# Optimization experiments

Hardware: AMD Instinct MI355X
Metric: run time of the kernel (lower is better)

Reference implementation:

```python
import jax, jax.numpy as jnp
import numpy as np

B, S, D, H = 2, 2048, 1024, 16
HD = D // H


def setup_inputs() -> dict:
    key = jax.random.key(0)
    ks = jax.random.split(key, 6)
    std = 1.0 / np.sqrt(D)
    return {
        "hidden_states": jax.random.normal(ks[0], (B, S, D), dtype=jnp.float32),
        "attention_mask": jnp.zeros((B, 1, S, S), dtype=jnp.float32),
        "Wq": jax.random.normal(ks[1], (D, D), dtype=jnp.float32) * std,
        "bq": jnp.zeros((D,), dtype=jnp.float32),
        "Wk": jax.random.normal(ks[2], (D, D), dtype=jnp.float32) * std,
        "bk": jnp.zeros((D,), dtype=jnp.float32),
        "Wv": jax.random.normal(ks[3], (D, D), dtype=jnp.float32) * std,
        "bv": jnp.zeros((D,), dtype=jnp.float32),
        "Wo": jax.random.normal(ks[4], (D, D), dtype=jnp.float32) * std,
        "bo": jnp.zeros((D,), dtype=jnp.float32),
    }


def reference(hidden_states, attention_mask, Wq, bq, Wk, bk, Wv, bv, Wo, bo):
    scale = HD ** (-0.5)
    # torch Linear: y = x @ W^T + b
    def proj(x, W, b):
        y = jnp.einsum('bsd,ed->bse', x, W) + b
        return y.reshape(B, S, H, HD).transpose(0, 2, 1, 3)  # [B,H,S,HD]
    q = proj(hidden_states, Wq, bq)
    k = proj(hidden_states, Wk, bk)
    v = proj(hidden_states, Wv, bv)
    scores = jnp.einsum('bhqd,bhkd->bhqk', q, k) * scale + attention_mask
    attn = jax.nn.softmax(scores, axis=-1)  # dropout p=0.0 -> identity
    out = jnp.einsum('bhqk,bhkd->bhqd', attn, v)
    out = out.transpose(0, 2, 1, 3).reshape(B, S, D)
    return jnp.einsum('bsd,ed->bse', out, Wo) + bo
```

## Files before the change

kernel.cpp:

```cpp
#include <hip/hip_runtime.h>
#include <hip/hip_bf16.h>
#include <stdint.h>

#define Bb 2
#define Ss 2048
#define Dd 1024
#define Hh 16
#define HD 64

typedef __attribute__((ext_vector_type(8))) __bf16 bf16x8;
typedef __attribute__((ext_vector_type(4))) __bf16 bf16x4;
typedef __attribute__((ext_vector_type(2))) __bf16 bf16x2;
typedef __attribute__((ext_vector_type(4))) float f32x4;
typedef __attribute__((ext_vector_type(16))) float f32x16;

#define LOG2E 1.44269504088896f
#define SCL2 (0.125f * LOG2E)

#define HS_N   (Bb * Ss * Dd)
#define W_N    (Dd * Dd)
#define B_N    (Dd)
#define MS_N   ((long)Bb * Ss * Ss)
#define CAN_HS 0
#define CAN_WQ (CAN_HS + HS_N)
#define CAN_BQ (CAN_WQ + W_N)
#define CAN_WK (CAN_BQ + B_N)
#define CAN_BK (CAN_WK + W_N)
#define CAN_WV (CAN_BK + B_N)
#define CAN_BV (CAN_WV + W_N)
#define CAN_WO (CAN_BV + B_N)
#define CAN_BO (CAN_WO + W_N)
#define CAN_END (CAN_BO + B_N)
#define TSZ    (Bb * Hh * Ss * HD)
#define WS_ELEMS (CAN_END + 4 * TSZ)
#define WS_NEED ((size_t)WS_ELEMS * 2)

__device__ __forceinline__ void gl_lds16(const __bf16* g, __bf16* l) {
  __builtin_amdgcn_global_load_lds(
      (const __attribute__((address_space(1))) void*)g,
      (__attribute__((address_space(3))) void*)l,
      16, 0, 0);
}

__device__ __forceinline__ void cfence() { asm volatile("" ::: "memory"); }

__global__ void canon_kernel(const float* hs, const float* Wq, const float* bq,
                             const float* Wk, const float* bk, const float* Wv,
                             const float* bv, const float* Wo, const float* bo,
                             __bf16* __restrict__ dst) {
  const float* srcs[9] = {hs, Wq, bq, Wk, bk, Wv, bv, Wo, bo};
  const long starts[10] = {CAN_HS, CAN_WQ, CAN_BQ, CAN_WK, CAN_BK,
                           CAN_WV, CAN_BV, CAN_WO, CAN_BO, CAN_END};
  const long nA = CAN_END / 8;
  for (long c = blockIdx.x * blockDim.x + threadIdx.x; c < nA;
       c += (long)gridDim.x * blockDim.x) {
    const long i = c * 8;
    int seg = 0;
#pragma unroll
    for (int t = 1; t < 9; t++) seg += (i >= starts[t]) ? 1 : 0;
    const float* s = srcs[seg] + (i - starts[seg]);
    bf16x8 v;
#pragma unroll
    for (int e = 0; e < 8; e++) v[e] = (__bf16)s[e];
    *(bf16x8*)(dst + i) = v;
  }
}

template <int MODE, typename OutT>
__global__ __launch_bounds__(256, 3) void gemm_bt(
    const __bf16* __restrict__ A,
    const __bf16* __restrict__ W0, const __bf16* __restrict__ W1,
    const __bf16* __restrict__ W2,
    const __bf16* __restrict__ b0, const __bf16* __restrict__ b1,
    const __bf16* __restrict__ b2,
    OutT* __restrict__ O0, OutT* __restrict__ O1, OutT* __restrict__ O2,
    const float* __restrict__ Mf, __bf16* __restrict__ Mout) {
  constexpr int TN = (MODE == 1) ? 64 : 128;
  constexpr int NACC = TN / 32;
  __shared__ __align__(16) __bf16 sA[2][128 * 32];
  __shared__ __align__(16) __bf16 sB[2][TN * 32];
  const int tid = threadIdx.x;

  if (MODE == 0 && blockIdx.y >= 24) {
    const long nC = MS_N / 8;
    const long c0 = ((long)(blockIdx.y - 24) * 32 + blockIdx.x) * 256 + tid;
    for (long c = c0; c < nC; c += 65536) {
      const float* s = Mf + c * 8;
      bf16x8 v;
#pragma unroll
      for (int e = 0; e < 8; e++) v[e] = (__bf16)(s[e] * LOG2E);
      *(bf16x8*)(Mout + c * 8) = v;
    }
    return;
  }

  const int lane = tid & 63;
  const int wid = tid >> 6;
  const int quad = lane >> 4;
  const int l15 = lane & 15;
  const int mBlock = blockIdx.x * 128;

  const __bf16* W;
  const __bf16* bias;
  OutT* Out;
  int nBlock, which = 0;
  if (MODE == 0) {
    which = blockIdx.y >> 3;
    nBlock = (blockIdx.y & 7) * 128;
    W = which == 0 ? W0 : (which == 1 ? W1 : W2);
    bias = which == 0 ? b0 : (which == 1 ? b1 : b2);
    Out = which == 0 ? O0 : (which == 1 ? O1 : O2);
  } else {
    nBlock = blockIdx.y * TN;
    W = W0;
    bias = b0;
    Out = O0;
  }

  const int waveM = (wid >> 1) * 64;
  const int waveN = (wid & 1) * (TN / 2);

  f32x4 acc[4][NACC] = {};

  const int c1 = wid * 64 + lane;
  const int c2 = c1 + 256;
  const __bf16* Ar1 = A + (mBlock + (c1 >> 2)) * Dd + (c1 & 3) * 8;
  const __bf16* Ar2 = A + (mBlock + (c2 >> 2)) * Dd + (c2 & 3) * 8;
  const __bf16* Wr1 = W + (nBlock + (c1 >> 2)) * Dd + (c1 & 3) * 8;
  const __bf16* Wr2 = W + (nBlock + (c2 >> 2)) * Dd + (c2 & 3) * 8;
  const int d1 = (wid * 64) * 8;
  const int d2 = (wid * 64 + 256) * 8;

#define GSTAGE(BI, K0)                                                        \
  {                                                                           \
    gl_lds16(Ar1 + (K0), sA[BI] + d1);                                        \
    gl_lds16(Ar2 + (K0), sA[BI] + d2);                                        \
    gl_lds16(Wr1 + (K0), sB[BI] + d1);                                        \
    if (MODE == 0) gl_lds16(Wr2 + (K0), sB[BI] + d2);                         \
  }

  GSTAGE(0, 0);

#pragma unroll 2
  for (int kt = 0; kt < 32; ++kt) {
    const int bufc = kt & 1;
    __syncthreads();
    if (kt < 31) {
      GSTAGE(bufc ^ 1, (kt + 1) * 32);
    }

    bf16x8 aF[4], bF[NACC];
#pragma unroll
    for (int mi = 0; mi < 4; mi++)
      aF[mi] =
          *(const bf16x8*)(sA[bufc] + (waveM + mi * 16 + l15) * 32 + quad * 8);
#pragma unroll
    for (int ni = 0; ni < NACC; ni++)
      bF[ni] =
          *(const bf16x8*)(sB[bufc] + (waveN + ni * 16 + l15) * 32 + quad * 8);
#pragma unroll
    for (int mi = 0; mi < 4; mi++)
#pragma unroll
      for (int ni = 0; ni < NACC; ni++)
        acc[mi][ni] = __builtin_amdgcn_mfma_f32_16x16x32_bf16(
            aF[mi], bF[ni], acc[mi][ni], 0, 0, 0);
  }

#pragma unroll
  for (int ni = 0; ni < NACC; ni++) {
    const int ng = nBlock + waveN + ni * 16 + l15;
    const float bv = (float)bias[ng];
#pragma unroll
    for (int mi = 0; mi < 4; mi++) {
      const int mg0 = mBlock + waveM + mi * 16 + quad * 4;
      if (MODE == 0 && which == 2) {
        const int b = mg0 >> 11, s0 = mg0 & 2047;
        const int h = ng >> 6, hd = ng & 63;
        bf16x4 pk;
#pragma unroll
        for (int r = 0; r < 4; r++) pk[r] = (__bf16)(acc[mi][ni][r] + bv);
        *(bf16x4*)((__bf16*)Out + (((b * Hh + h) * HD + hd) * Ss) + s0) = pk;
      } else {
#pragma unroll
        for (int r = 0; r < 4; r++) {
          float v = acc[mi][ni][r] + bv;
          const int m = mg0 + r;
          if (MODE == 0) {
            if (which == 0) v *= SCL2;
            const int b = m >> 11, s = m & 2047;
            const int h = ng >> 6, hd = ng & 63;
            Out[(((b * Hh + h) * Ss + s) * HD) + hd] = (OutT)v;
          } else {
            Out[m * Dd + ng] = (OutT)v;
          }
        }
      }
    }
  }
}

__global__ __launch_bounds__(256, 4) void attn_fused(
    const __bf16* __restrict__ Qg, const __bf16* __restrict__ Kg,
    const __bf16* __restrict__ Vt, const __bf16* __restrict__ Mbf,
    __bf16* __restrict__ Og) {
  __shared__ __align__(16) union {
    struct {
      __bf16 kv[2][8192];
      __bf16 mk[4096];
    } s;
    struct {
      float O[2][64][32];
      float L[2][32];
    } m;
  } sh;

  const int tid = threadIdx.x;
  const int lane = tid & 63;
  const int wid = tid >> 6;
  const int qg = wid & 1;
  const int kvh = wid >> 1;
  const int l31 = lane & 31;
  const int hi = lane >> 5;

  const int id = blockIdx.x;
  const int j = id >> 3;
  const int bh = (id & 7) * 4 + (j >> 5);
  const int qb0 = (j & 31) * 64;
  const int b = bh >> 4;
  const int h = bh & 15;
  const int qw = qb0 + qg * 32 + l31;

  const __bf16* Qp = Qg + (size_t)bh * Ss * HD;
  const __bf16* Kp = Kg + (size_t)bh * Ss * HD;
  const __bf16* Vp = Vt + (size_t)bh * HD * Ss;
  const __bf16* Mb = Mbf + (size_t)b * Ss * Ss;

  bf16x8 qf[4];
#pragma unroll
  for (int k = 0; k < 4; k++)
    qf[k] = *(const bf16x8*)(Qp + (size_t)qw * HD + k * 16 + hi * 8);

  const int cA = tid, cB = 256 + tid;
#define STAGE_KV(BI, KVS)                                                     \
  {                                                                           \
    const int rwA = (cA & 255) >> 2, rwB = (cB & 255) >> 2;                   \
    const int slA = (cA & 3) ^ ((rwA >> 1) & 3);                              \
    const int slB = (cB & 3) ^ ((rwB >> 1) & 3);                              \
    __bf16* kb = sh.s.kv[BI];                                                 \
    gl_lds16(Kp + ((KVS) + rwA) * HD + (cA >> 8) * 32 + slA * 8, kb + cA * 8);\
    gl_lds16(Kp + ((KVS) + rwB) * HD + (cB >> 8) * 32 + slB * 8, kb + cB * 8);\
    __bf16* vb = sh.s.kv[BI] + 4096;                                          \
    gl_lds16(Vp + (size_t)rwA * Ss + (KVS) + (cA >> 8) * 32 + slA * 8,        \
             vb + cA * 8);                                                    \
    gl_lds16(Vp + (size_t)rwB * Ss + (KVS) + (cB >> 8) * 32 + slB * 8,        \
             vb + cB * 8);                                                    \
  }

#define STAGE_M(KVS)                                                          \
  {                                                                           \
    _Pragma("unroll")                                                         \
    for (int rr = 0; rr < 2; rr++) {                                          \
      const int c = tid + rr * 256;                                           \
      const int mq = c >> 3;                                                  \
      const int l8 = (c & 7) ^ (mq & 7);                                      \
      gl_lds16(Mb + (size_t)(qb0 + mq) * Ss + (KVS) + l8 * 8,                 \
               sh.s.mk + c * 8);                                              \
    }                                                                         \
  }

  f32x16 o[2] = {};
  f32x4 lacc = {0.f, 0.f, 0.f, 0.f};

  const int rsw = (l31 >> 1) & 3;

  STAGE_KV(0, 0);
  STAGE_M(0);

  for (int it = 0; it < 32; ++it) {
    const int bufc = it & 1;
    cfence();
    asm volatile("s_waitcnt vmcnt(0)" ::: "memory");
    cfence();
    __builtin_amdgcn_s_barrier();
    cfence();
    if (it < 31) {
      STAGE_KV(bufc ^ 1, (it + 1) * 64);
      cfence();
    }

    bf16x4 mcv[4];
    const int mq = qg * 32 + l31;
#pragma unroll
    for (int g = 0; g < 4; g++) {
      const int p8 = (4 * kvh + g) ^ (l31 & 7);
      mcv[g] = *(const bf16x4*)(sh.s.mk + mq * 64 + p8 * 8 + 4 * hi);
    }
    cfence();
    asm volatile("s_waitcnt lgkmcnt(0)" ::: "memory");
    cfence();
    __builtin_amdgcn_s_barrier();
    cfence();
    if (it < 31) {
      STAGE_M((it + 1) * 64);
      cfence();
    }

    f32x16 sacc;
#pragma unroll
    for (int g = 0; g < 4; g++)
#pragma unroll
      for (int r = 0; r < 4; r++) sacc[g * 4 + r] = (float)mcv[g][r];
    __builtin_amdgcn_s_setprio(1);
#pragma unroll
    for (int k = 0; k < 4; k++) {
      const int ps = (((k & 1) << 1) | hi) ^ rsw;
      bf16x8 kf = *(const bf16x8*)(sh.s.kv[bufc] +
                                   ((k >> 1) * 64 + kvh * 32 + l31) * 32 +
                                   ps * 8);
      sacc = __builtin_amdgcn_mfma_f32_32x32x16_bf16(kf, qf[k], sacc, 0, 0, 0);
    }
    __builtin_amdgcn_s_setprio(0);

    f32x4 sv[4];
#pragma unroll
    for (int g = 0; g < 4; g++)
#pragma unroll
      for (int r = 0; r < 4; r++)
        sv[g][r] = __builtin_amdgcn_exp2f(sacc[g * 4 + r]);
    lacc += (sv[0] + sv[1]) + (sv[2] + sv[3]);

    union pu { bf16x4 v; uint32_t w[2]; };
    pu pk[4];
#pragma unroll
    for (int g = 0; g < 4; g++)
#pragma unroll
      for (int r = 0; r < 4; r++) pk[g].v[r] = (__bf16)sv[g][r];
    union PF { bf16x8 v; uint32_t u[4]; } pf[2];
#pragma unroll
    for (int ks = 0; ks < 2; ks++) {
      uint32_t a0 = pk[2 * ks].w[0], b0 = pk[2 * ks + 1].w[0];
      uint32_t a1 = pk[2 * ks].w[1], b1 = pk[2 * ks + 1].w[1];
      asm volatile("s_nop 1\n\tv_permlane32_swap_b32 %0, %1"
                   : "+v"(a0), "+v"(b0));
      asm volatile("s_nop 1\n\tv_permlane32_swap_b32 %0, %1"
                   : "+v"(a1), "+v"(b1));
      pf[ks].u[0] = a0;
      pf[ks].u[1] = a1;
      pf[ks].u[2] = b0;
      pf[ks].u[3] = b1;
    }

    __builtin_amdgcn_s_setprio(1);
#pragma unroll
    for (int k = 0; k < 2; k++)
#pragma unroll
      for (int hb = 0; hb < 2; hb++) {
        const int ps = ((k << 1) | hi) ^ rsw;
        bf16x8 vf = *(const bf16x8*)(sh.s.kv[bufc] + 4096 +
                                     (kvh * 64 + hb * 32 + l31) * 32 +
                                     ps * 8);
        o[hb] = __builtin_amdgcn_mfma_f32_32x32x16_bf16(vf, pf[k].v, o[hb],
                                                        0, 0, 0);
      }
    __builtin_amdgcn_s_setprio(0);
  }

  float l = lacc[0] + lacc[1] + lacc[2] + lacc[3];
  l += __shfl_xor(l, 32);

  __syncthreads();
  if (kvh == 1) {
#pragma unroll
    for (int hb = 0; hb < 2; hb++)
#pragma unroll
      for (int r = 0; r < 16; r++) {
        const int hd = hb * 32 + (r & 3) + 8 * (r >> 2) + 4 * hi;
        sh.m.O[qg][hd][l31] = o[hb][r];
      }
    if (hi == 0) sh.m.L[qg][l31] = l;
  }
  __syncthreads();
  if (kvh == 0) {
#pragma unroll
    for (int hb = 0; hb < 2; hb++)
#pragma unroll
      for (int r = 0; r < 16; r++) {
        const int hd = hb * 32 + (r & 3) + 8 * (r >> 2) + 4 * hi;
        o[hb][r] += sh.m.O[qg][hd][l31];
      }
    l += sh.m.L[qg][l31];
    const float inv = 1.0f / l;
    __bf16* Ow = Og + (((size_t)b * Ss + qw) * Hh + h) * HD;
#pragma unroll
    for (int hb = 0; hb < 2; hb++)
#pragma unroll
      for (int g = 0; g < 4; g++) {
        const int hd = hb * 32 + g * 8 + 4 * hi;
        bf16x2 w0, w1;
        w0[0] = (__bf16)(o[hb][g * 4 + 0] * inv);
        w0[1] = (__bf16)(o[hb][g * 4 + 1] * inv);
        w1[0] = (__bf16)(o[hb][g * 4 + 2] * inv);
        w1[1] = (__bf16)(o[hb][g * 4 + 3] * inv);
        *(bf16x2*)(Ow + hd) = w0;
        *(bf16x2*)(Ow + hd + 2) = w1;
      }
  }
}

extern "C" void kernel_launch(void* const* d_in, const int* in_sizes, int n_in,
                              void* d_out, int out_size, void* d_ws,
                              size_t ws_size, hipStream_t stream) {
  if (ws_size < WS_NEED) return;

  __bf16* ws = (__bf16*)d_ws;
  const __bf16* hsC = ws + CAN_HS;
  const __bf16* WqC = ws + CAN_WQ;
  const __bf16* bqC = ws + CAN_BQ;
  const __bf16* WkC = ws + CAN_WK;
  const __bf16* bkC = ws + CAN_BK;
  const __bf16* WvC = ws + CAN_WV;
  const __bf16* bvC = ws + CAN_BV;
  const __bf16* WoC = ws + CAN_WO;
  const __bf16* boC = ws + CAN_BO;
  __bf16* Q = ws + CAN_END;
  __bf16* K = Q + TSZ;
  __bf16* V = K + TSZ;
  __bf16* AW = V + TSZ;
  float* out = (float*)d_out;
  __bf16* Mbf = (__bf16*)d_out;

  canon_kernel<<<2048, 256, 0, stream>>>(
      (const float*)d_in[0], (const float*)d_in[2], (const float*)d_in[3],
      (const float*)d_in[4], (const float*)d_in[5], (const float*)d_in[6],
      (const float*)d_in[7], (const float*)d_in[8], (const float*)d_in[9], ws);
  gemm_bt<0, __bf16><<<dim3(32, 32), 256, 0, stream>>>(
      hsC, WqC, WkC, WvC, bqC, bkC, bvC, Q, K, V, (const float*)d_in[1], Mbf);
  gemm_bt<0, __bf16><<<dim3(32, 24), 256, 0, stream>>>(
      hsC, WqC, WkC, WvC, bqC, bkC, bvC, Q, K, V, (const float*)d_in[1], Mbf);
  attn_fused<<<dim3(1024), 256, 0, stream>>>(Q, K, V, Mbf, AW);
  gemm_bt<1, float><<<dim3(32, 16), 256, 0, stream>>>(
      AW, WoC, WoC, WoC, boC, boC, boC, out, out, out, nullptr, nullptr);
}
```

Baseline: 265.0 us.

## Pre-tile mask into MFMA fragment order and load it directly to registers

The mask conversion now writes the bf16 mask in a per-tile layout that matches each lane's MFMA accumulator fragment. The attention kernel can then load its mask values with two vector global loads per iteration, prefetched one tile ahead, instead of staging them through LDS. This removes the LDS mask buffer, one barrier and an lgkmcnt wait per iteration. A redundant second launch of the QKV projection kernel is also removed. The trade-off is more registers for the prefetched mask and scattered writes in the conversion kernel.

```diff
diff --git a/kernel.cpp b/kernel.cpp
--- a/kernel.cpp
+++ b/kernel.cpp
@@ -85,11 +85,23 @@
     const long nC = MS_N / 8;
     const long c0 = ((long)(blockIdx.y - 24) * 32 + blockIdx.x) * 256 + tid;
     for (long c = c0; c < nC; c += 65536) {
-      const float* s = Mf + c * 8;
-      bf16x8 v;
-#pragma unroll
-      for (int e = 0; e < 8; e++) v[e] = (__bf16)(s[e] * LOG2E);
-      *(bf16x8*)(Mout + c * 8) = v;
+      const long i = c * 8;
+      const int b = (int)(i >> 22);
+      const int q = (int)((i >> 11) & 2047);
+      const int kv = (int)(i & 2047);
+      const float* s = Mf + i;
+      const int qt = q >> 6, qg = (q >> 5) & 1, l31 = q & 31;
+      const int kvt = kv >> 6, kvh = (kv >> 5) & 1, g = (kv >> 3) & 3;
+      const long tb = ((long)((b * 32 + qt) * 32 + kvt)) << 12;
+      const int t0 = (kvh << 7) | (qg << 6) | l31;
+      bf16x4 w0, w1;
+#pragma unroll
+      for (int r = 0; r < 4; r++) {
+        w0[r] = (__bf16)(s[r] * LOG2E);
+        w1[r] = (__bf16)(s[4 + r] * LOG2E);
+      }
+      *(bf16x4*)(Mout + tb + t0 * 16 + g * 4) = w0;
+      *(bf16x4*)(Mout + tb + (t0 + 32) * 16 + g * 4) = w1;
     }
     return;
   }
@@ -204,10 +216,7 @@
     const __bf16* __restrict__ Vt, const __bf16* __restrict__ Mbf,
     __bf16* __restrict__ Og) {
   __shared__ __align__(16) union {
-    struct {
-      __bf16 kv[2][8192];
-      __bf16 mk[4096];
-    } s;
+    __bf16 kv[2][8192];
     struct {
       float O[2][64][32];
       float L[2][32];
@@ -225,7 +234,8 @@
   const int id = blockIdx.x;
   const int j = id >> 3;
   const int bh = (id & 7) * 4 + (j >> 5);
-  const int qb0 = (j & 31) * 64;
+  const int qt = j & 31;
+  const int qb0 = qt * 64;
   const int b = bh >> 4;
   const int h = bh & 15;
   const int qw = qb0 + qg * 32 + l31;
@@ -233,7 +243,7 @@
   const __bf16* Qp = Qg + (size_t)bh * Ss * HD;
   const __bf16* Kp = Kg + (size_t)bh * Ss * HD;
   const __bf16* Vp = Vt + (size_t)bh * HD * Ss;
-  const __bf16* Mb = Mbf + (size_t)b * Ss * Ss;
+  const __bf16* Mt = Mbf + (((long)(b * 32 + qt) * 32) << 12) + tid * 16;
 
   bf16x8 qf[4];
 #pragma unroll
@@ -246,35 +256,24 @@
     const int rwA = (cA & 255) >> 2, rwB = (cB & 255) >> 2;                   \
     const int slA = (cA & 3) ^ ((rwA >> 1) & 3);                              \
     const int slB = (cB & 3) ^ ((rwB >> 1) & 3);                              \
-    __bf16* kb = sh.s.kv[BI];                                                 \
+    __bf16* kb = sh.kv[BI];                                                   \
     gl_lds16(Kp + ((KVS) + rwA) * HD + (cA >> 8) * 32 + slA * 8, kb + cA * 8);\
     gl_lds16(Kp + ((KVS) + rwB) * HD + (cB >> 8) * 32 + slB * 8, kb + cB * 8);\
-    __bf16* vb = sh.s.kv[BI] + 4096;                                          \
+    __bf16* vb = sh.kv[BI] + 4096;                                            \
     gl_lds16(Vp + (size_t)rwA * Ss + (KVS) + (cA >> 8) * 32 + slA * 8,        \
              vb + cA * 8);                                                    \
     gl_lds16(Vp + (size_t)rwB * Ss + (KVS) + (cB >> 8) * 32 + slB * 8,        \
              vb + cB * 8);                                                    \
   }
 
-#define STAGE_M(KVS)                                                          \
-  {                                                                           \
-    _Pragma("unroll")                                                         \
-    for (int rr = 0; rr < 2; rr++) {                                          \
-      const int c = tid + rr * 256;                                           \
-      const int mq = c >> 3;                                                  \
-      const int l8 = (c & 7) ^ (mq & 7);                                      \
-      gl_lds16(Mb + (size_t)(qb0 + mq) * Ss + (KVS) + l8 * 8,                 \
-               sh.s.mk + c * 8);                                              \
-    }                                                                         \
-  }
-
   f32x16 o[2] = {};
   f32x4 lacc = {0.f, 0.f, 0.f, 0.f};
 
   const int rsw = (l31 >> 1) & 3;
 
   STAGE_KV(0, 0);
-  STAGE_M(0);
+  bf16x8 mc0 = *(const bf16x8*)(Mt);
+  bf16x8 mc1 = *(const bf16x8*)(Mt + 8);
 
   for (int it = 0; it < 32; ++it) {
     const int bufc = it & 1;
@@ -283,38 +282,26 @@
     cfence();
     __builtin_amdgcn_s_barrier();
     cfence();
+    bf16x8 mn0, mn1;
     if (it < 31) {
       STAGE_KV(bufc ^ 1, (it + 1) * 64);
       cfence();
-    }
-
-    bf16x4 mcv[4];
-    const int mq = qg * 32 + l31;
-#pragma unroll
-    for (int g = 0; g < 4; g++) {
-      const int p8 = (4 * kvh + g) ^ (l31 & 7);
-      mcv[g] = *(const bf16x4*)(sh.s.mk + mq * 64 + p8 * 8 + 4 * hi);
-    }
-    cfence();
-    asm volatile("s_waitcnt lgkmcnt(0)" ::: "memory");
-    cfence();
-    __builtin_amdgcn_s_barrier();
-    cfence();
-    if (it < 31) {
-      STAGE_M((it + 1) * 64);
+      mn0 = *(const bf16x8*)(Mt + (it + 1) * 4096);
+      mn1 = *(const bf16x8*)(Mt + (it + 1) * 4096 + 8);
       cfence();
     }
 
     f32x16 sacc;
 #pragma unroll
-    for (int g = 0; g < 4; g++)
-#pragma unroll
-      for (int r = 0; r < 4; r++) sacc[g * 4 + r] = (float)mcv[g][r];
+    for (int e = 0; e < 8; e++) {
+      sacc[e] = (float)mc0[e];
+      sacc[8 + e] = (float)mc1[e];
+    }
     __builtin_amdgcn_s_setprio(1);
 #pragma unroll
     for (int k = 0; k < 4; k++) {
       const int ps = (((k & 1) << 1) | hi) ^ rsw;
-      bf16x8 kf = *(const bf16x8*)(sh.s.kv[bufc] +
+      bf16x8 kf = *(const bf16x8*)(sh.kv[bufc] +
                                    ((k >> 1) * 64 + kvh * 32 + l31) * 32 +
                                    ps * 8);
       sacc = __builtin_amdgcn_mfma_f32_32x32x16_bf16(kf, qf[k], sacc, 0, 0, 0);
@@ -356,13 +343,16 @@
 #pragma unroll
       for (int hb = 0; hb < 2; hb++) {
         const int ps = ((k << 1) | hi) ^ rsw;
-        bf16x8 vf = *(const bf16x8*)(sh.s.kv[bufc] + 4096 +
+        bf16x8 vf = *(const bf16x8*)(sh.kv[bufc] + 4096 +
                                      (kvh * 64 + hb * 32 + l31) * 32 +
                                      ps * 8);
         o[hb] = __builtin_amdgcn_mfma_f32_32x32x16_bf16(vf, pf[k].v, o[hb],
                                                         0, 0, 0);
       }
     __builtin_amdgcn_s_setprio(0);
+
+    mc0 = mn0;
+    mc1 = mn1;
   }
 
   float l = lacc[0] + lacc[1] + lacc[2] + lacc[3];
@@ -435,8 +425,6 @@
       (const float*)d_in[7], (const float*)d_in[8], (const float*)d_in[9], ws);
   gemm_bt<0, __bf16><<<dim3(32, 32), 256, 0, stream>>>(
       hsC, WqC, WkC, WvC, bqC, bkC, bvC, Q, K, V, (const float*)d_in[1], Mbf);
-  gemm_bt<0, __bf16><<<dim3(32, 24), 256, 0, stream>>>(
-      hsC, WqC, WkC, WvC, bqC, bkC, bvC, Q, K, V, (const float*)d_in[1], Mbf);
   attn_fused<<<dim3(1024), 256, 0, stream>>>(Q, K, V, Mbf, AW);
   gemm_bt<1, float><<<dim3(32, 16), 256, 0, stream>>>(
       AW, WoC, WoC, WoC, boC, boC, boC, out, out, out, nullptr, nullptr);
```

Result: faster. 233.6 us (-11.9%).
